# Kernel optimization log

Measured on AMD Instinct MI355X. Metric: run time of the kernel, lower is better.

## Reference

```python
import jax, jax.numpy as jnp
import numpy as np

NUM_EMBED = 1024
EMBED_DIM = 256
COMMIT_COEF = 0.25


def setup_inputs() -> dict:
    key = jax.random.key(0)
    k1, k2 = jax.random.split(key)
    input = jax.random.normal(k1, (16, EMBED_DIM, 64, 64), dtype=jnp.float32)
    codebook = jax.random.normal(k2, (NUM_EMBED, EMBED_DIM), dtype=jnp.float32)
    last_used = jnp.zeros((NUM_EMBED,), dtype=jnp.int32)
    return {"input": input, "codebook": codebook, "last_used": last_used}


def reference(input, codebook, last_used):
    # (B, D, H, W) -> (B, H, W, D) -> (N, D)
    x = jnp.moveaxis(input, 1, -1)
    batch_shape = x.shape[:-1]
    flat = x.reshape(-1, x.shape[-1])  # (N, D)

    # Squared euclidean distances; argmin is identical to argmin of torch.cdist
    # (monotone sqrt), computed as a GEMM for efficiency.
    d2 = (
        jnp.sum(flat * flat, axis=-1, keepdims=True)
        - 2.0 * (flat @ codebook.T)
        + jnp.sum(codebook * codebook, axis=-1)
    )  # (N, K)
    idxes = jnp.argmin(d2, axis=-1).reshape(batch_shape)  # (B, H, W)

    embed = codebook[idxes]                 # (B, H, W, D) gather
    embed = jnp.moveaxis(embed, -1, 1)      # (B, D, H, W)

    # replace_unused bookkeeping (scatter). With last_used starting at zero,
    # last_used >= replace_after never triggers, so no codebook rewrite occurs.
    is_used = jnp.zeros((NUM_EMBED,), dtype=bool).at[idxes.ravel()].set(True)
    new_last_used = jnp.where(is_used, jnp.int32(0), last_used + jnp.int32(1))

    sg = jax.lax.stop_gradient
    codebook_loss = jnp.mean((sg(embed) - input) ** 2)
    commitment_loss = jnp.mean((embed - sg(input)) ** 2)
    vq_loss = codebook_loss + COMMIT_COEF * commitment_loss

    return idxes, embed, vq_loss, new_last_used
```

## Files before the change

### kernel.cpp

```cpp
#include <hip/hip_runtime.h>

#define NUM_EMBED 1024
#define EMBED_DIM 256
#define SPATIAL 4096
#define NROWS 65536
#define EMBED_ELEMS 16777216
#define HMARGIN 0.05f

typedef _Float16 half8 __attribute__((ext_vector_type(8)));
typedef float f32x4 __attribute__((ext_vector_type(4)));

__device__ __forceinline__ unsigned fkey(float f) {
  unsigned u = __float_as_uint(f);
  return (u & 0x80000000u) ? ~u : (u | 0x80000000u);
}

__device__ __forceinline__ void gll16(const _Float16* g, void* l) {
  __builtin_amdgcn_global_load_lds((const __attribute__((address_space(1))) void*)g,
                                   (__attribute__((address_space(3))) void*)l, 16, 0, 0);
}

#define UPD(V1, V2, I1, S, I)                            \
  { float _s = (S);                                      \
    if (_s < (V1)) { (V2) = (V1); (V1) = _s; (I1) = (I); } \
    else if (_s < (V2)) { (V2) = _s; } }

#define MERGE(V1A, V2A, I1A, V1B, V2B, I1B)                       \
  { if ((V1B) < (V1A)) { (V2A) = fminf((V1A), (V2B)); (V1A) = (V1B); (I1A) = (I1B); } \
    else { (V2A) = fminf((V2A), (V1B)); } }

__global__ __launch_bounds__(256) void k_init(const float* __restrict__ cb,
                                              int* __restrict__ used,
                                              int* __restrict__ flagcount,
                                              float* __restrict__ cnorm,
                                              _Float16* __restrict__ cb16) {
  int bid = blockIdx.x, tid = threadIdx.x;
  if (bid == 0) {
    used[tid] = 0; used[tid + 256] = 0; used[tid + 512] = 0; used[tid + 768] = 0;
    if (tid == 0) *flagcount = 0;
  } else if (bid <= 64) {
    int c = (bid - 1) * 16 + (tid >> 4);
    int l = tid & 15;
    const float4* p = (const float4*)(cb + c * EMBED_DIM + l * 16);
    float s = 0.f;
#pragma unroll
    for (int j = 0; j < 4; ++j) {
      float4 v = p[j];
      s += v.x * v.x + v.y * v.y + v.z * v.z + v.w * v.w;
    }
#pragma unroll
    for (int off = 1; off < 16; off <<= 1) s += __shfl_xor(s, off, 16);
    if (l == 0) cnorm[c] = s;
  } else {
    int gid = (bid - 65) * 256 + tid;
    int ch = gid >> 9;
    int rem = gid & 511;
    int ks = rem >> 6;
    int lg = (rem >> 4) & 3;
    int ln = rem & 15;
    int S = (ch * 16 + ln) * 256 + ks * 32 + lg * 8;
    const float4* src = (const float4*)(cb + S);
    float4 a = src[0], b = src[1];
    half8 h;
    h[0] = (_Float16)a.x; h[1] = (_Float16)a.y; h[2] = (_Float16)a.z; h[3] = (_Float16)a.w;
    h[4] = (_Float16)b.x; h[5] = (_Float16)b.y; h[6] = (_Float16)b.z; h[7] = (_Float16)b.w;
    *(half8*)(cb16 + gid * 8) = h;
  }
}

__global__ __launch_bounds__(256, 2) void k_score(const float* __restrict__ in,
                                                  const _Float16* __restrict__ cb16,
                                                  const float* __restrict__ cnorm,
                                                  float* __restrict__ out_idx,
                                                  int* __restrict__ idxi,
                                                  int* __restrict__ flagged,
                                                  int* __restrict__ flagcount,
                                                  int* __restrict__ used) {
  __shared__ _Float16 As[8][4096];
  __shared__ float cn_lds[1024];
  int tid = threadIdx.x;
  int lane = tid & 63;
  int wave = tid >> 6;
  int ln = lane & 15;
  int lg = lane >> 4;
  int r0 = blockIdx.x << 6;
  const float* Ain = in + ((r0 >> 12) * (EMBED_DIM * SPATIAL)) + (r0 & 4095);

  {
    char* scratch = (char*)As[0];
    int row = tid & 63;
    int kq = tid >> 6;
    const float* p0 = Ain + row;
#pragma unroll
    for (int j = 0; j < 8; ++j) {
      int kc = kq * 8 + j;
      half8 hv;
#pragma unroll
      for (int q = 0; q < 8; ++q) hv[q] = (_Float16)p0[(kc * 8 + q) * SPATIAL];
      *(half8*)(scratch + kc * 1024 + row * 16) = hv;
    }
#pragma unroll
    for (int i = 0; i < 4; ++i) cn_lds[tid + 256 * i] = 0.5f * cnorm[tid + 256 * i];
  }
  __syncthreads();
  half8 xf[8][4];
  {
    const char* scratch = (const char*)As[0];
#pragma unroll
    for (int ks = 0; ks < 8; ++ks)
#pragma unroll
      for (int nf = 0; nf < 4; ++nf)
        xf[ks][nf] = *(const half8*)(scratch + (ks * 4 + lg) * 1024 + (nf * 16 + ln) * 16);
  }
  __syncthreads();

  char* ring = (char*)As[0] + wave * 16384;
  const _Float16* src0 = cb16 + wave * 65536 + lane * 8;

#pragma unroll
  for (int i = 0; i < 8; ++i) gll16(src0 + i * 512, ring + i * 1024 + lane * 16);

  float sv1[4] = {3e38f, 3e38f, 3e38f, 3e38f};
  float sv2[4] = {3e38f, 3e38f, 3e38f, 3e38f};
  int si1[4] = {0, 0, 0, 0};
  int afo = lg * 256 + ln * 16;

#pragma unroll 1
  for (int c = 0; c < 16; ++c) {
    if (c < 15) {
      char* dst = ring + ((c + 1) & 1) * 8192;
      const _Float16* ps = src0 + (c + 1) * 4096;
#pragma unroll
      for (int i = 0; i < 8; ++i) gll16(ps + i * 512, dst + i * 1024 + lane * 16);
      asm volatile("s_waitcnt vmcnt(8)" ::: "memory");
    } else {
      asm volatile("s_waitcnt vmcnt(0)" ::: "memory");
    }
    __builtin_amdgcn_sched_barrier(0);
    const char* Ac = ring + (c & 1) * 8192;
    f32x4 acc[4] = {};
    __builtin_amdgcn_s_setprio(1);
#pragma unroll
    for (int ks = 0; ks < 8; ++ks) {
      half8 af = *(const half8*)(Ac + ks * 1024 + afo);
#pragma unroll
      for (int nf = 0; nf < 4; ++nf)
        acc[nf] = __builtin_amdgcn_mfma_f32_16x16x32_f16(af, xf[ks][nf], acc[nf], 0, 0, 0);
    }
    __builtin_amdgcn_s_setprio(0);
    int cb0 = wave * 256 + c * 16;
    float cna[4];
    *(float4*)cna = *(const float4*)(cn_lds + cb0 + lg * 4);
    int ib0 = cb0 + lg * 4;
#pragma unroll
    for (int nf = 0; nf < 4; ++nf) {
      float v1a = cna[0] - acc[nf][0], v2a = 3e38f;
      int i1a = ib0;
#pragma unroll
      for (int r = 1; r < 4; ++r) UPD(v1a, v2a, i1a, cna[r] - acc[nf][r], ib0 + r);
      MERGE(sv1[nf], sv2[nf], si1[nf], v1a, v2a, i1a);
    }
  }

#pragma unroll
  for (int nf = 0; nf < 4; ++nf) {
#pragma unroll
    for (int off = 16; off < 64; off <<= 1) {
      float ov1 = __shfl_xor(sv1[nf], off);
      float ov2 = __shfl_xor(sv2[nf], off);
      int oi = __shfl_xor(si1[nf], off);
      if (ov1 < sv1[nf]) { sv2[nf] = fminf(sv1[nf], ov2); sv1[nf] = ov1; si1[nf] = oi; }
      else { sv2[nf] = fminf(sv2[nf], ov1); }
    }
  }

  __syncthreads();
  float* mv1 = (float*)As[0];
  float* mv2 = mv1 + 256;
  int* mi1 = (int*)(mv2 + 256);
  if (lg == 0) {
#pragma unroll
    for (int nf = 0; nf < 4; ++nf) {
      int slot = wave * 64 + nf * 16 + ln;
      mv1[slot] = sv1[nf]; mv2[slot] = sv2[nf]; mi1[slot] = si1[nf];
    }
  }
  __syncthreads();
  if (tid < 64) {
    float v1 = mv1[tid], v2 = mv2[tid];
    int i1 = mi1[tid];
#pragma unroll
    for (int w = 1; w < 4; ++w)
      MERGE(v1, v2, i1, mv1[w * 64 + tid], mv2[w * 64 + tid], mi1[w * 64 + tid]);
    int grow = r0 + tid;
    out_idx[grow] = (float)i1;
    idxi[grow] = i1;
    if (v2 - v1 < HMARGIN) {
      int p = atomicAdd(flagcount, 1);
      flagged[p] = grow;
    } else {
      used[i1] = 1;
    }
  }
}

__global__ __launch_bounds__(256) void k_cleanup(const float* __restrict__ in,
                                                 const float* __restrict__ cb,
                                                 const float* __restrict__ cnorm,
                                                 const int* __restrict__ flagged,
                                                 const int* __restrict__ flagcount,
                                                 float* __restrict__ out_idx,
                                                 int* __restrict__ idxi,
                                                 int* __restrict__ used) {
  __shared__ float xs[256];
  __shared__ unsigned long long red[4];
  int tid = threadIdx.x;
  int lane = tid & 63;
  int wave = tid >> 6;
  int sub = lane & 15;
  int cg = lane >> 4;
  int nf = *flagcount;
  const float4* cb4 = (const float4*)cb;
  for (int fi = blockIdx.x; fi < nf; fi += 2048) {
    int row = flagged[fi];
    int b = row >> 12, s = row & 4095;
    xs[tid] = in[b * (EMBED_DIM * SPATIAL) + tid * SPATIAL + s];
    __syncthreads();
    const float4* xs4 = (const float4*)xs;
    float4 x0 = xs4[sub], x1 = xs4[16 + sub], x2 = xs4[32 + sub], x3 = xs4[48 + sub];
    unsigned long long best = ~0ull;
    int c0 = wave * 256 + cg;
#pragma unroll 4
    for (int g = 0; g < 64; ++g) {
      int c = c0 + g * 4;
      const float4* crow = cb4 + c * 64 + sub;
      float4 d0 = crow[0], d1 = crow[16], d2 = crow[32], d3 = crow[48];
      float p = d0.x * x0.x + d0.y * x0.y + d0.z * x0.z + d0.w * x0.w;
      p += d1.x * x1.x + d1.y * x1.y + d1.z * x1.z + d1.w * x1.w;
      p += d2.x * x2.x + d2.y * x2.y + d2.z * x2.z + d2.w * x2.w;
      p += d3.x * x3.x + d3.y * x3.y + d3.z * x3.z + d3.w * x3.w;
#pragma unroll
      for (int off = 1; off < 16; off <<= 1) p += __shfl_xor(p, off);
      if (sub == 0) {
        float sc = cnorm[c] - 2.0f * p;
        unsigned long long k = ((unsigned long long)fkey(sc) << 32) | (unsigned)c;
        best = k < best ? k : best;
      }
    }
    {
      unsigned long long o = __shfl_xor(best, 16); best = o < best ? o : best;
      o = __shfl_xor(best, 32); best = o < best ? o : best;
    }
    if (lane == 0) red[wave] = best;
    __syncthreads();
    if (tid == 0) {
      unsigned long long bb = red[0];
#pragma unroll
      for (int w = 1; w < 4; ++w) { unsigned long long o = red[w]; bb = o < bb ? o : bb; }
      int idx = (int)(bb & 0xffffffffull);
      out_idx[row] = (float)idx;
      idxi[row] = idx;
      used[idx] = 1;
    }
    __syncthreads();
  }
}

__global__ __launch_bounds__(256) void k_gather(const float* __restrict__ in,
                                                const float* __restrict__ cb,
                                                const int* __restrict__ idxi,
                                                float* __restrict__ embed_out,
                                                double* __restrict__ partials) {
  __shared__ float E[64][257];
  __shared__ int idx_l[64];
  __shared__ float wsum[4];
  int tid = threadIdx.x;
  int lane = tid & 63;
  int wave = tid >> 6;
  int r0 = blockIdx.x << 6;
  int b = r0 >> 12;
  int s0 = r0 & 4095;
  if (tid < 64) idx_l[tid] = idxi[r0 + tid];
  __syncthreads();
  const float4* cb4 = (const float4*)cb;
#pragma unroll
  for (int jj = 0; jj < 16; ++jj) {
    int j = wave * 16 + jj;
    float4 v = cb4[idx_l[j] * 64 + lane];
    E[j][lane * 4 + 0] = v.x;
    E[j][lane * 4 + 1] = v.y;
    E[j][lane * 4 + 2] = v.z;
    E[j][lane * 4 + 3] = v.w;
  }
  __syncthreads();
  float lsum = 0.f;
  int dbase = wave * 64;
  const float* inp = in + (b * EMBED_DIM + dbase) * SPATIAL + s0;
  float* outp = embed_out + (b * EMBED_DIM + dbase) * SPATIAL + s0;
#pragma unroll 8
  for (int dd = 0; dd < 64; ++dd) {
    float e = E[lane][dbase + dd];
    float x = inp[dd * SPATIAL + lane];
    outp[dd * SPATIAL + lane] = e;
    float df = e - x;
    lsum += df * df;
  }
#pragma unroll
  for (int off = 1; off < 64; off <<= 1) lsum += __shfl_xor(lsum, off, 64);
  if (lane == 0) wsum[wave] = lsum;
  __syncthreads();
  if (tid == 0)
    partials[blockIdx.x] = (double)(wsum[0] + wsum[1] + wsum[2] + wsum[3]);
}

__global__ __launch_bounds__(256) void k_tail(const double* __restrict__ partials,
                                              const int* __restrict__ used,
                                              const int* __restrict__ last_used,
                                              float* __restrict__ out_loss,
                                              float* __restrict__ out_lu) {
  int tid = threadIdx.x;
  double s = 0.0;
  for (int i = tid; i < 1024; i += 256) s += partials[i];
#pragma unroll
  for (int off = 1; off < 64; off <<= 1) s += __shfl_xor(s, off, 64);
  __shared__ double sd[4];
  if ((tid & 63) == 0) sd[tid >> 6] = s;
  __syncthreads();
  if (tid == 0) {
    double total = sd[0] + sd[1] + sd[2] + sd[3];
    out_loss[0] = (float)(1.25 * total / (double)EMBED_ELEMS);
  }
  for (int i = tid; i < NUM_EMBED; i += 256)
    out_lu[i] = used[i] ? 0.0f : (float)(last_used[i] + 1);
}

extern "C" void kernel_launch(void* const* d_in, const int* in_sizes, int n_in,
                              void* d_out, int out_size, void* d_ws, size_t ws_size,
                              hipStream_t stream) {
  const float* in = (const float*)d_in[0];
  const float* cb = (const float*)d_in[1];
  const int* last_used = (const int*)d_in[2];

  float* out = (float*)d_out;
  float* out_idx = out;
  float* embed_out = out + NROWS;
  float* out_loss = embed_out + EMBED_ELEMS;
  float* out_lu = out_loss + 1;

  _Float16* cb16 = (_Float16*)d_ws;
  double* partials = (double*)(cb16 + NUM_EMBED * EMBED_DIM);
  int* flagged = (int*)(partials + 4096);
  int* flagcount = flagged + NROWS;
  int* idxi = flagcount + 16;
  int* used = idxi + NROWS;
  float* cnorm = (float*)(used + NUM_EMBED);

  hipLaunchKernelGGL(k_init, dim3(193), dim3(256), 0, stream, cb, used, flagcount, cnorm, cb16);
  hipLaunchKernelGGL(k_score, dim3(1024), dim3(256), 0, stream, in, cb16, cnorm, out_idx,
                     idxi, flagged, flagcount, used);
  hipLaunchKernelGGL(k_cleanup, dim3(2048), dim3(256), 0, stream, in, cb, cnorm, flagged,
                     flagcount, out_idx, idxi, used);
  hipLaunchKernelGGL(k_gather, dim3(1024), dim3(256), 0, stream, in, cb, idxi, embed_out,
                     partials);
  hipLaunchKernelGGL(k_tail, dim3(1), dim3(256), 0, stream, partials, used, last_used,
                     out_loss, out_lu);
}
```

Before: 136.0 us.

## Stage codebook tiles through registers and halve gather rows per block

In the scoring kernel, the double-buffered direct global-to-LDS codebook loads are replaced by register staging into a single per-wave LDS buffer. Each chunk's load is issued before the MFMA work and written to LDS after the argmin update, which halves the kernel's LDS footprint to allow more resident blocks. The gather/loss kernel now handles 32 rows per block over twice as many blocks, with lanes split across two embedding dimensions, to cut its LDS use and raise occupancy. The trade-offs are more VGPR pressure in the scoring kernel next to its large register-resident input fragments, and narrower contiguous global segments per half-wave in the gather.

```diff
diff --git a/kernel.cpp b/kernel.cpp
--- a/kernel.cpp
+++ b/kernel.cpp
@@ -13,11 +13,6 @@
 __device__ __forceinline__ unsigned fkey(float f) {
   unsigned u = __float_as_uint(f);
   return (u & 0x80000000u) ? ~u : (u | 0x80000000u);
-}
-
-__device__ __forceinline__ void gll16(const _Float16* g, void* l) {
-  __builtin_amdgcn_global_load_lds((const __attribute__((address_space(1))) void*)g,
-                                   (__attribute__((address_space(3))) void*)l, 16, 0, 0);
 }
 
 #define UPD(V1, V2, I1, S, I)                            \
@@ -76,7 +71,7 @@
                                                   int* __restrict__ flagged,
                                                   int* __restrict__ flagcount,
                                                   int* __restrict__ used) {
-  __shared__ _Float16 As[8][4096];
+  __shared__ _Float16 As[4][4096];
   __shared__ float cn_lds[1024];
   int tid = threadIdx.x;
   int lane = tid & 63;
@@ -114,11 +109,14 @@
   }
   __syncthreads();
 
-  char* ring = (char*)As[0] + wave * 16384;
+  char* buf = (char*)As[0] + wave * 8192;
   const _Float16* src0 = cb16 + wave * 65536 + lane * 8;
 
-#pragma unroll
-  for (int i = 0; i < 8; ++i) gll16(src0 + i * 512, ring + i * 1024 + lane * 16);
+  half8 stg[8];
+#pragma unroll
+  for (int i = 0; i < 8; ++i) stg[i] = *(const half8*)(src0 + i * 512);
+#pragma unroll
+  for (int i = 0; i < 8; ++i) *(half8*)(buf + i * 1024 + lane * 16) = stg[i];
 
   float sv1[4] = {3e38f, 3e38f, 3e38f, 3e38f};
   float sv2[4] = {3e38f, 3e38f, 3e38f, 3e38f};
@@ -128,21 +126,15 @@
 #pragma unroll 1
   for (int c = 0; c < 16; ++c) {
     if (c < 15) {
-      char* dst = ring + ((c + 1) & 1) * 8192;
       const _Float16* ps = src0 + (c + 1) * 4096;
 #pragma unroll
-      for (int i = 0; i < 8; ++i) gll16(ps + i * 512, dst + i * 1024 + lane * 16);
-      asm volatile("s_waitcnt vmcnt(8)" ::: "memory");
-    } else {
-      asm volatile("s_waitcnt vmcnt(0)" ::: "memory");
-    }
-    __builtin_amdgcn_sched_barrier(0);
-    const char* Ac = ring + (c & 1) * 8192;
+      for (int i = 0; i < 8; ++i) stg[i] = *(const half8*)(ps + i * 512);
+    }
     f32x4 acc[4] = {};
     __builtin_amdgcn_s_setprio(1);
 #pragma unroll
     for (int ks = 0; ks < 8; ++ks) {
-      half8 af = *(const half8*)(Ac + ks * 1024 + afo);
+      half8 af = *(const half8*)(buf + ks * 1024 + afo);
 #pragma unroll
       for (int nf = 0; nf < 4; ++nf)
         acc[nf] = __builtin_amdgcn_mfma_f32_16x16x32_f16(af, xf[ks][nf], acc[nf], 0, 0, 0);
@@ -159,6 +151,10 @@
 #pragma unroll
       for (int r = 1; r < 4; ++r) UPD(v1a, v2a, i1a, cna[r] - acc[nf][r], ib0 + r);
       MERGE(sv1[nf], sv2[nf], si1[nf], v1a, v2a, i1a);
+    }
+    if (c < 15) {
+#pragma unroll
+      for (int i = 0; i < 8; ++i) *(half8*)(buf + i * 1024 + lane * 16) = stg[i];
     }
   }
 
@@ -271,21 +267,21 @@
                                                 const int* __restrict__ idxi,
                                                 float* __restrict__ embed_out,
                                                 double* __restrict__ partials) {
-  __shared__ float E[64][257];
-  __shared__ int idx_l[64];
+  __shared__ float E[32][257];
+  __shared__ int idx_l[32];
   __shared__ float wsum[4];
   int tid = threadIdx.x;
   int lane = tid & 63;
   int wave = tid >> 6;
-  int r0 = blockIdx.x << 6;
+  int r0 = blockIdx.x << 5;
   int b = r0 >> 12;
   int s0 = r0 & 4095;
-  if (tid < 64) idx_l[tid] = idxi[r0 + tid];
+  if (tid < 32) idx_l[tid] = idxi[r0 + tid];
   __syncthreads();
   const float4* cb4 = (const float4*)cb;
 #pragma unroll
-  for (int jj = 0; jj < 16; ++jj) {
-    int j = wave * 16 + jj;
+  for (int jj = 0; jj < 8; ++jj) {
+    int j = wave * 8 + jj;
     float4 v = cb4[idx_l[j] * 64 + lane];
     E[j][lane * 4 + 0] = v.x;
     E[j][lane * 4 + 1] = v.y;
@@ -294,14 +290,16 @@
   }
   __syncthreads();
   float lsum = 0.f;
-  int dbase = wave * 64;
-  const float* inp = in + (b * EMBED_DIM + dbase) * SPATIAL + s0;
-  float* outp = embed_out + (b * EMBED_DIM + dbase) * SPATIAL + s0;
+  int s = lane & 31;
+  int dpar = lane >> 5;
+  const float* inp = in + b * (EMBED_DIM * SPATIAL) + s0 + s;
+  float* outp = embed_out + b * (EMBED_DIM * SPATIAL) + s0 + s;
 #pragma unroll 8
-  for (int dd = 0; dd < 64; ++dd) {
-    float e = E[lane][dbase + dd];
-    float x = inp[dd * SPATIAL + lane];
-    outp[dd * SPATIAL + lane] = e;
+  for (int i = 0; i < 32; ++i) {
+    int d = wave * 64 + i * 2 + dpar;
+    float e = E[s][d];
+    float x = inp[d * SPATIAL];
+    outp[d * SPATIAL] = e;
     float df = e - x;
     lsum += df * df;
   }
@@ -320,7 +318,7 @@
                                               float* __restrict__ out_lu) {
   int tid = threadIdx.x;
   double s = 0.0;
-  for (int i = tid; i < 1024; i += 256) s += partials[i];
+  for (int i = tid; i < 2048; i += 256) s += partials[i];
 #pragma unroll
   for (int off = 1; off < 64; off <<= 1) s += __shfl_xor(s, off, 64);
   __shared__ double sd[4];
@@ -360,7 +358,7 @@
                      idxi, flagged, flagcount, used);
   hipLaunchKernelGGL(k_cleanup, dim3(2048), dim3(256), 0, stream, in, cb, cnorm, flagged,
                      flagcount, out_idx, idxi, used);
-  hipLaunchKernelGGL(k_gather, dim3(1024), dim3(256), 0, stream, in, cb, idxi, embed_out,
+  hipLaunchKernelGGL(k_gather, dim3(2048), dim3(256), 0, stream, in, cb, idxi, embed_out,
                      partials);
   hipLaunchKernelGGL(k_tail, dim3(1), dim3(256), 0, stream, partials, used, last_used,
                      out_loss, out_lu);
```

Measured after the change: 133.4 us. Within noise of the previous version (-1.9%).
